# Kernel tuning notes

Hardware: AMD Instinct MI355X
Metric: run time of the kernel (lower is better)

Reference implementation:

```python
import jax, jax.numpy as jnp
import numpy as np

N = 50000   # nodes
E = 800000  # edges (avg degree 16)
D = 128     # feature dim
H = 4       # heads
DH = D // H # head dim


def setup_inputs() -> dict:
    key = jax.random.key(0)
    ks = jax.random.split(key, 12)
    s = 1.0 / np.sqrt(D)
    return {
        "x": jax.random.normal(ks[0], (N, D), dtype=jnp.float32),
        "src": jax.random.randint(ks[1], (E,), 0, N, dtype=jnp.int32),
        "dst": jax.random.randint(ks[2], (E,), 0, N, dtype=jnp.int32),
        # input_linear: Linear(d, d)
        "W_in": jax.random.uniform(ks[3], (D, D), jnp.float32, -s, s),
        "b_in": jax.random.uniform(ks[4], (D,), jnp.float32, -s, s),
        # attn_linear_u: Linear(d, n_heads), attn_linear_v: Linear(d, n_heads, bias=False)
        "W_au": jax.random.uniform(ks[5], (D, H), jnp.float32, -s, s),
        "b_au": jax.random.uniform(ks[6], (H,), jnp.float32, -s, s),
        "W_av": jax.random.uniform(ks[7], (D, H), jnp.float32, -s, s),
        # FFN: Linear(d, d) -> ReLU -> Linear(d, d)  (dropout=0)
        "W_f1": jax.random.uniform(ks[8], (D, D), jnp.float32, -s, s),
        "b_f1": jax.random.uniform(ks[9], (D,), jnp.float32, -s, s),
        "W_f2": jax.random.uniform(ks[10], (D, D), jnp.float32, -s, s),
        "b_f2": jax.random.uniform(ks[11], (D,), jnp.float32, -s, s),
    }


def reference(x, src, dst, W_in, b_in, W_au, b_au, W_av, W_f1, b_f1, W_f2, b_f2):
    h = x @ W_in + b_in                                # [N, D]
    su = h @ W_au + b_au                               # [N, H]
    sv = h @ W_av                                      # [N, H]
    # u_add_v gather + LeakyReLU
    e = jax.nn.leaky_relu(su[src] + sv[dst], 0.2)      # [E, H]
    # edge_softmax: softmax over incoming edges of each dst node
    m = jax.ops.segment_max(e, dst, num_segments=N)    # [N, H]
    ex = jnp.exp(e - m[dst])                           # [E, H]
    z = jax.ops.segment_sum(ex, dst, num_segments=N)   # [N, H]
    p = ex / z[dst]                                    # [E, H]
    # u_mul_e_sum: weighted aggregation (note reshape order (N, d_head, H))
    hu = h.reshape(N, DH, H)[src]                      # [E, DH, H]
    agg = jax.ops.segment_sum(hu * p[:, None, :], dst, num_segments=N)  # [N, DH, H]
    y = agg.reshape(N, D)
    # FFN
    return jax.nn.relu(y @ W_f1 + b_f1) @ W_f2 + b_f2
```

## Files before the change

kernel.cpp:

```cpp
#include <hip/hip_runtime.h>
#include <hip/hip_bf16.h>
#include <math.h>

#define D 128
#define NHEADS 4

static constexpr int CAP  = 64;
static constexpr int CAPB = 5120;
static constexpr int EB   = 4096;

typedef __attribute__((ext_vector_type(8))) short bf16x8;
typedef __attribute__((ext_vector_type(4))) float f32x4;

__device__ __forceinline__ float4 ld4(const float* p) {
    return *reinterpret_cast<const float4*>(p);
}
__device__ __forceinline__ float4 fma4(float a, float4 b, float4 c) {
    c.x = fmaf(a, b.x, c.x); c.y = fmaf(a, b.y, c.y);
    c.z = fmaf(a, b.z, c.z); c.w = fmaf(a, b.w, c.w);
    return c;
}
__device__ __forceinline__ unsigned short f2bf(float f) {
    __hip_bfloat16 b = __float2bfloat16(f);
    return __builtin_bit_cast(unsigned short, b);
}
__device__ __forceinline__ float bf2f(unsigned short u) {
    return __uint_as_float((unsigned)u << 16);
}
__device__ __forceinline__ void cvt_hilo(const float4& a0, const float4& a1,
                                         bf16x8& hi, bf16x8& lo) {
    float v[8] = {a0.x, a0.y, a0.z, a0.w, a1.x, a1.y, a1.z, a1.w};
#pragma unroll
    for (int i = 0; i < 8; ++i) {
        unsigned short h = f2bf(v[i]);
        hi[i] = (short)h;
        lo[i] = (short)f2bf(v[i] - bf2f(h));
    }
}

template<int MODE>
__global__ __launch_bounds__(256)
void mfma_gemm128(const float* __restrict__ A, const float* __restrict__ W,
                  const float* __restrict__ bias, float* __restrict__ out,
                  unsigned short* __restrict__ out16, int N, int ntiles,
                  const float* __restrict__ Wau, const float* __restrict__ bau,
                  const float* __restrict__ Wav,
                  float* __restrict__ su, float* __restrict__ sv)
{
    __shared__ unsigned short wh[D * D];
    __shared__ unsigned short wl[D * D];

    const int t = threadIdx.x;
#pragma unroll
    for (int i = 0; i < 16; ++i) {
        int g = t + i * 256;
        int col = g & 127;
        int k0 = (g >> 7) << 2;
        short4 h4, l4;
#pragma unroll
        for (int k = 0; k < 4; ++k) {
            float v = W[(size_t)(k0 + k) * D + col];
            unsigned short hb = f2bf(v);
            ((short*)&h4)[k] = (short)hb;
            ((short*)&l4)[k] = (short)f2bf(v - bf2f(hb));
        }
        int off = col * D + (k0 ^ ((col & 7) << 3));
        *reinterpret_cast<short4*>(&wh[off]) = h4;
        *reinterpret_cast<short4*>(&wl[off]) = l4;
    }
    __syncthreads();

    const int wid  = t >> 6;
    const int lane = t & 63;
    const int q8   = (lane >> 4) * 8;

    float4 bau4 = {0, 0, 0, 0};
    if constexpr (MODE == 0) bau4 = ld4(bau);

    for (int tile = blockIdx.x; tile < ntiles; tile += gridDim.x) {
        const int rbase = tile * 64 + wid * 16;
        const int arow  = rbase + (lane & 15);

        bf16x8 ahi[4], alo[4];
#pragma unroll
        for (int ks = 0; ks < 4; ++ks) {
            float4 a0 = {0, 0, 0, 0}, a1 = {0, 0, 0, 0};
            if (arow < N) {
                const float* ap = A + (size_t)arow * D + 32 * ks + q8;
                a0 = ld4(ap); a1 = ld4(ap + 4);
            }
            cvt_hilo(a0, a1, ahi[ks], alo[ks]);
        }

        f32x4 acc[8];
#pragma unroll
        for (int ct = 0; ct < 8; ++ct) acc[ct] = (f32x4){0.f, 0.f, 0.f, 0.f};

#pragma unroll
        for (int ct = 0; ct < 8; ++ct) {
            const int colb = ct * 16 + (lane & 15);
            const int sw   = (colb & 7) << 3;
            bf16x8 bh[4], bl[4];
#pragma unroll
            for (int ks = 0; ks < 4; ++ks) {
                int off = colb * D + ((32 * ks + q8) ^ sw);
                bh[ks] = *reinterpret_cast<const bf16x8*>(&wh[off]);
                bl[ks] = *reinterpret_cast<const bf16x8*>(&wl[off]);
            }
#pragma unroll
            for (int ks = 0; ks < 4; ++ks) {
                acc[ct] = __builtin_amdgcn_mfma_f32_16x16x32_bf16(ahi[ks], bh[ks], acc[ct], 0, 0, 0);
                acc[ct] = __builtin_amdgcn_mfma_f32_16x16x32_bf16(alo[ks], bh[ks], acc[ct], 0, 0, 0);
                acc[ct] = __builtin_amdgcn_mfma_f32_16x16x32_bf16(ahi[ks], bl[ks], acc[ct], 0, 0, 0);
            }
        }

        const int crow0 = rbase + (lane >> 4) * 4;

        float4 s_u[4], s_v[4];
        if constexpr (MODE == 0) {
#pragma unroll
            for (int j = 0; j < 4; ++j) { s_u[j] = {0,0,0,0}; s_v[j] = {0,0,0,0}; }
        }

#pragma unroll
        for (int ct = 0; ct < 8; ++ct) {
            const int col = ct * 16 + (lane & 15);
            const float bv = bias[col];
            float4 wau4, wav4;
            if constexpr (MODE == 0) {
                wau4 = ld4(Wau + col * NHEADS);
                wav4 = ld4(Wav + col * NHEADS);
            }
#pragma unroll
            for (int j = 0; j < 4; ++j) {
                const int r = crow0 + j;
                float v = acc[ct][j] + bv;
                if constexpr (MODE == 1) v = fmaxf(v, 0.f);
                if (r < N) {
                    if constexpr (MODE == 0)
                        out16[(size_t)r * D + col] = f2bf(v);
                    else
                        out[(size_t)r * D + col] = v;
                }
                if constexpr (MODE == 0) {
                    s_u[j] = fma4(v, wau4, s_u[j]);
                    s_v[j] = fma4(v, wav4, s_v[j]);
                }
            }
        }

        if constexpr (MODE == 0) {
#pragma unroll
            for (int j = 0; j < 4; ++j) {
#pragma unroll
                for (int d2 = 1; d2 < 16; d2 <<= 1) {
                    s_u[j].x += __shfl_xor(s_u[j].x, d2); s_u[j].y += __shfl_xor(s_u[j].y, d2);
                    s_u[j].z += __shfl_xor(s_u[j].z, d2); s_u[j].w += __shfl_xor(s_u[j].w, d2);
                    s_v[j].x += __shfl_xor(s_v[j].x, d2); s_v[j].y += __shfl_xor(s_v[j].y, d2);
                    s_v[j].z += __shfl_xor(s_v[j].z, d2); s_v[j].w += __shfl_xor(s_v[j].w, d2);
                }
            }
            if ((lane & 15) == 0) {
#pragma unroll
                for (int j = 0; j < 4; ++j) {
                    const int r = crow0 + j;
                    if (r < N) {
                        float4 u = s_u[j];
                        u.x += bau4.x; u.y += bau4.y; u.z += bau4.z; u.w += bau4.w;
                        *reinterpret_cast<float4*>(su + (size_t)r * NHEADS) = u;
                        *reinterpret_cast<float4*>(sv + (size_t)r * NHEADS) = s_v[j];
                    }
                }
            }
        }
    }
}

__global__ __launch_bounds__(256)
void bin_kernel(const int* __restrict__ src, const int* __restrict__ dst,
                int* __restrict__ bucket_cnt ,
                unsigned* __restrict__ bucket_buf, int E, int NB)
{
    __shared__ int hist[256];
    __shared__ int base[256];
    __shared__ int off[256];
    const int t = threadIdx.x;
    hist[t] = 0; off[t] = 0;
    __syncthreads();

    const int e0 = blockIdx.x * EB;
#pragma unroll
    for (int j = 0; j < EB / 256; ++j) {
        int idx = e0 + j * 256 + t;
        if (idx < E) atomicAdd(&hist[dst[idx] >> 8], 1);
    }
    __syncthreads();
    if (t < NB) {
        int hv = hist[t];
        base[t] = hv ? atomicAdd(&bucket_cnt[t * 16], hv) : 0;
    }
    __syncthreads();
#pragma unroll
    for (int j = 0; j < EB / 256; ++j) {
        int idx = e0 + j * 256 + t;
        if (idx < E) {
            int d = dst[idx];
            int b = d >> 8;
            int p = base[b] + atomicAdd(&off[b], 1);
            if (p < CAPB)
                bucket_buf[(size_t)b * CAPB + p] =
                    (unsigned)(src[idx] | ((d & 255) << 16));
        }
    }
}

__global__ __launch_bounds__(256)
void csr_kernel(const int* __restrict__ bucket_cnt, const unsigned* __restrict__ bucket_buf,
                unsigned short* __restrict__ slot, int* __restrict__ deg, int N)
{
    __shared__ unsigned ebuf[CAPB];
    __shared__ int cur[256];
    const int b = blockIdx.x;
    const int t = threadIdx.x;
    const int cnt = min(bucket_cnt[b * 16], CAPB);
    cur[t] = 0;
    for (int i = t; i < cnt; i += 256)
        ebuf[i] = bucket_buf[(size_t)b * CAPB + i];
    __syncthreads();
    for (int i = t; i < cnt; i += 256) {
        unsigned e = ebuf[i];
        int dl = e >> 16;
        int pos = atomicAdd(&cur[dl], 1);
        if (pos < CAP)
            slot[(((size_t)(b * 256 + dl)) << 6) + pos] = (unsigned short)(e & 0xffff);
    }
    __syncthreads();
    int n = b * 256 + t;
    if (n < N) deg[n] = min(cur[t], CAP);
}

__global__ __launch_bounds__(256)
void agg_kernel(const unsigned short* __restrict__ h16, const float* __restrict__ su,
                const float* __restrict__ sv, const int* __restrict__ deg_arr,
                const unsigned short* __restrict__ slot, float* __restrict__ y, int N)
{
    __shared__ int   s_s[4][64];
    __shared__ float s_p[4][64][4];

    const int wslot = threadIdx.x >> 6;
    const int lane  = threadIdx.x & 63;
    const int n = blockIdx.x * 4 + wslot;
    if (n >= N) return;

    const int deg = deg_arr[n];

    if (deg == 0) {
        *reinterpret_cast<float2*>(y + (size_t)n * D + lane * 2) = float2{0.f, 0.f};
        return;
    }

    const float4 sv4 = ld4(sv + (size_t)n * NHEADS);

    float4 z4 = {0.f, 0.f, 0.f, 0.f};
    float2 acc = {0.f, 0.f};
    const int psel = (lane & 1) * 2;

    int sj = 0;
    float4 ex4 = {0.f, 0.f, 0.f, 0.f};
    if (lane < deg) {
        sj = slot[((size_t)n << 6) + lane];
        float4 u = ld4(su + (size_t)sj * NHEADS);
        float e0 = u.x + sv4.x, e1 = u.y + sv4.y, e2 = u.z + sv4.z, e3 = u.w + sv4.w;
        e0 = e0 >= 0.f ? e0 : 0.2f * e0; e1 = e1 >= 0.f ? e1 : 0.2f * e1;
        e2 = e2 >= 0.f ? e2 : 0.2f * e2; e3 = e3 >= 0.f ? e3 : 0.2f * e3;
        ex4.x = __expf(e0); ex4.y = __expf(e1);
        ex4.z = __expf(e2); ex4.w = __expf(e3);
    }
    float4 tt = ex4;
#pragma unroll
    for (int d2 = 1; d2 < 64; d2 <<= 1) {
        tt.x += __shfl_xor(tt.x, d2); tt.y += __shfl_xor(tt.y, d2);
        tt.z += __shfl_xor(tt.z, d2); tt.w += __shfl_xor(tt.w, d2);
    }
    z4.x += tt.x; z4.y += tt.y; z4.z += tt.z; z4.w += tt.w;

    s_s[wslot][lane] = sj;
    *reinterpret_cast<float4*>(&s_p[wslot][lane][0]) = ex4;
    __builtin_amdgcn_wave_barrier();

#pragma unroll 4
    for (int j = 0; j < deg; ++j) {
        int s = s_s[wslot][j];
        float2 p2 = *reinterpret_cast<const float2*>(&s_p[wslot][j][psel]);
        unsigned u = *reinterpret_cast<const unsigned*>(h16 + ((size_t)s << 7) + (lane << 1));
        acc.x = fmaf(p2.x, __uint_as_float(u << 16), acc.x);
        acc.y = fmaf(p2.y, __uint_as_float(u & 0xffff0000u), acc.y);
    }

    const float2 z2 = (lane & 1) ? float2{z4.z, z4.w} : float2{z4.x, z4.y};
    float2 o;
    o.x = acc.x / z2.x;
    o.y = acc.y / z2.y;
    *reinterpret_cast<float2*>(y + (size_t)n * D + lane * 2) = o;
}

extern "C" void kernel_launch(void* const* d_in, const int* in_sizes, int n_in,
                              void* d_out, int out_size, void* d_ws, size_t ws_size,
                              hipStream_t stream) {
    const float* x    = (const float*)d_in[0];
    const int*   src  = (const int*)d_in[1];
    const int*   dst  = (const int*)d_in[2];
    const float* W_in = (const float*)d_in[3];
    const float* b_in = (const float*)d_in[4];
    const float* W_au = (const float*)d_in[5];
    const float* b_au = (const float*)d_in[6];
    const float* W_av = (const float*)d_in[7];
    const float* W_f1 = (const float*)d_in[8];
    const float* b_f1 = (const float*)d_in[9];
    const float* W_f2 = (const float*)d_in[10];
    const float* b_f2 = (const float*)d_in[11];
    float* out = (float*)d_out;

    const int N = in_sizes[0] / D;
    const int E = in_sizes[1];
    const int NB = (N + 255) / 256;

    char* ws = (char*)d_ws;
    size_t o = 0;
    auto alloc = [&](size_t bytes) -> void* {
        void* p = ws + o;
        o += (bytes + 255) & ~(size_t)255;
        return p;
    };
    void*           bufA       = alloc((size_t)N * D * 4);
    float*          y          = (float*)alloc((size_t)N * D * 4);
    float*          su         = (float*)alloc((size_t)N * NHEADS * 4);
    float*          sv         = (float*)alloc((size_t)N * NHEADS * 4);
    int*            bucket_cnt = (int*)alloc((size_t)NB * 16 * 4);
    unsigned*       bucket_buf = (unsigned*)alloc((size_t)NB * CAPB * 4);
    unsigned short* slot       = (unsigned short*)alloc((size_t)NB * 256 * CAP * 2);
    int*            deg        = (int*)alloc((size_t)N * 4);

    unsigned short* h16 = (unsigned short*)bufA;
    float*          hid = (float*)bufA;

    hipMemsetAsync(bucket_cnt, 0, (size_t)NB * 16 * 4, stream);

    const int ntiles = (N + 63) / 64;
    const int ggrid  = (ntiles + 1) / 2;
    const int bgrid  = (E + EB - 1) / EB;

    bin_kernel<<<bgrid, 256, 0, stream>>>(src, dst, bucket_cnt, bucket_buf, E, NB);

    mfma_gemm128<0><<<ggrid, 256, 0, stream>>>(x, W_in, b_in, nullptr, h16, N, ntiles,
                                               W_au, b_au, W_av, su, sv);

    csr_kernel<<<NB, 256, 0, stream>>>(bucket_cnt, bucket_buf, slot, deg, N);

    agg_kernel<<<(N + 3) / 4, 256, 0, stream>>>(h16, su, sv, deg, slot, y, N);

    mfma_gemm128<1><<<ggrid, 256, 0, stream>>>(y, W_f1, b_f1, hid, nullptr, N, ntiles,
                                               nullptr, nullptr, nullptr, nullptr, nullptr);
    mfma_gemm128<2><<<ggrid, 256, 0, stream>>>(hid, W_f2, b_f2, out, nullptr, N, ntiles,
                                               nullptr, nullptr, nullptr, nullptr, nullptr);
}
```

Baseline: 134.8 us.

## Precompute bf16 hi/lo weight splits once and split attention scores into separate kernel

```diff
diff --git a/kernel.cpp b/kernel.cpp
--- a/kernel.cpp
+++ b/kernel.cpp
@@ -38,18 +38,14 @@
     }
 }
 
-template<int MODE>
-__global__ __launch_bounds__(256)
-void mfma_gemm128(const float* __restrict__ A, const float* __restrict__ W,
-                  const float* __restrict__ bias, float* __restrict__ out,
-                  unsigned short* __restrict__ out16, int N, int ntiles,
-                  const float* __restrict__ Wau, const float* __restrict__ bau,
-                  const float* __restrict__ Wav,
-                  float* __restrict__ su, float* __restrict__ sv)
-{
-    __shared__ unsigned short wh[D * D];
-    __shared__ unsigned short wl[D * D];
-
+__global__ __launch_bounds__(256)
+void wprep_kernel(const float* __restrict__ W0, const float* __restrict__ W1,
+                  const float* __restrict__ W2, unsigned short* __restrict__ wpre)
+{
+    const float* Ws[3] = {W0, W1, W2};
+    const float* W = Ws[blockIdx.x];
+    unsigned short* oh = wpre + (size_t)blockIdx.x * 32768;
+    unsigned short* ol = oh + 16384;
     const int t = threadIdx.x;
 #pragma unroll
     for (int i = 0; i < 16; ++i) {
@@ -65,8 +61,31 @@
             ((short*)&l4)[k] = (short)f2bf(v - bf2f(hb));
         }
         int off = col * D + (k0 ^ ((col & 7) << 3));
-        *reinterpret_cast<short4*>(&wh[off]) = h4;
-        *reinterpret_cast<short4*>(&wl[off]) = l4;
+        *reinterpret_cast<short4*>(&oh[off]) = h4;
+        *reinterpret_cast<short4*>(&ol[off]) = l4;
+    }
+}
+
+template<int MODE>
+__global__ __launch_bounds__(256)
+void mfma_gemm128(const float* __restrict__ A, const unsigned short* __restrict__ wpre,
+                  const float* __restrict__ bias, float* __restrict__ out,
+                  unsigned short* __restrict__ out16, int N)
+{
+    __shared__ unsigned short wh[D * D];
+    __shared__ unsigned short wl[D * D];
+
+    const int t = threadIdx.x;
+    {
+        const float4* srcf = reinterpret_cast<const float4*>(wpre);
+        float4* dh = reinterpret_cast<float4*>(wh);
+        float4* dl = reinterpret_cast<float4*>(wl);
+#pragma unroll
+        for (int i = 0; i < 8; ++i) {
+            int idx = t + i * 256;
+            dh[idx] = srcf[idx];
+            dl[idx] = srcf[idx + 2048];
+        }
     }
     __syncthreads();
 
@@ -74,106 +93,97 @@
     const int lane = t & 63;
     const int q8   = (lane >> 4) * 8;
 
-    float4 bau4 = {0, 0, 0, 0};
-    if constexpr (MODE == 0) bau4 = ld4(bau);
-
-    for (int tile = blockIdx.x; tile < ntiles; tile += gridDim.x) {
-        const int rbase = tile * 64 + wid * 16;
-        const int arow  = rbase + (lane & 15);
-
-        bf16x8 ahi[4], alo[4];
+    const int rbase = blockIdx.x * 64 + wid * 16;
+    const int arow  = rbase + (lane & 15);
+
+    bf16x8 ahi[4], alo[4];
+#pragma unroll
+    for (int ks = 0; ks < 4; ++ks) {
+        float4 a0 = {0, 0, 0, 0}, a1 = {0, 0, 0, 0};
+        if (arow < N) {
+            const float* ap = A + (size_t)arow * D + 32 * ks + q8;
+            a0 = ld4(ap); a1 = ld4(ap + 4);
+        }
+        cvt_hilo(a0, a1, ahi[ks], alo[ks]);
+    }
+
+    f32x4 acc[8];
+#pragma unroll
+    for (int ct = 0; ct < 8; ++ct) acc[ct] = (f32x4){0.f, 0.f, 0.f, 0.f};
+
+#pragma unroll
+    for (int ct = 0; ct < 8; ++ct) {
+        const int colb = ct * 16 + (lane & 15);
+        const int sw   = (colb & 7) << 3;
+        bf16x8 bh[4], bl[4];
 #pragma unroll
         for (int ks = 0; ks < 4; ++ks) {
-            float4 a0 = {0, 0, 0, 0}, a1 = {0, 0, 0, 0};
-            if (arow < N) {
-                const float* ap = A + (size_t)arow * D + 32 * ks + q8;
-                a0 = ld4(ap); a1 = ld4(ap + 4);
-            }
-            cvt_hilo(a0, a1, ahi[ks], alo[ks]);
-        }
-
-        f32x4 acc[8];
-#pragma unroll
-        for (int ct = 0; ct < 8; ++ct) acc[ct] = (f32x4){0.f, 0.f, 0.f, 0.f};
-
-#pragma unroll
-        for (int ct = 0; ct < 8; ++ct) {
-            const int colb = ct * 16 + (lane & 15);
-            const int sw   = (colb & 7) << 3;
-            bf16x8 bh[4], bl[4];
-#pragma unroll
-            for (int ks = 0; ks < 4; ++ks) {
-                int off = colb * D + ((32 * ks + q8) ^ sw);
-                bh[ks] = *reinterpret_cast<const bf16x8*>(&wh[off]);
-                bl[ks] = *reinterpret_cast<const bf16x8*>(&wl[off]);
-            }
-#pragma unroll
-            for (int ks = 0; ks < 4; ++ks) {
-                acc[ct] = __builtin_amdgcn_mfma_f32_16x16x32_bf16(ahi[ks], bh[ks], acc[ct], 0, 0, 0);
-                acc[ct] = __builtin_amdgcn_mfma_f32_16x16x32_bf16(alo[ks], bh[ks], acc[ct], 0, 0, 0);
-                acc[ct] = __builtin_amdgcn_mfma_f32_16x16x32_bf16(ahi[ks], bl[ks], acc[ct], 0, 0, 0);
-            }
-        }
-
-        const int crow0 = rbase + (lane >> 4) * 4;
-
-        float4 s_u[4], s_v[4];
-        if constexpr (MODE == 0) {
-#pragma unroll
-            for (int j = 0; j < 4; ++j) { s_u[j] = {0,0,0,0}; s_v[j] = {0,0,0,0}; }
-        }
-
-#pragma unroll
-        for (int ct = 0; ct < 8; ++ct) {
-            const int col = ct * 16 + (lane & 15);
-            const float bv = bias[col];
-            float4 wau4, wav4;
-            if constexpr (MODE == 0) {
-                wau4 = ld4(Wau + col * NHEADS);
-                wav4 = ld4(Wav + col * NHEADS);
-            }
-#pragma unroll
-            for (int j = 0; j < 4; ++j) {
-                const int r = crow0 + j;
+            int off = colb * D + ((32 * ks + q8) ^ sw);
+            bh[ks] = *reinterpret_cast<const bf16x8*>(&wh[off]);
+            bl[ks] = *reinterpret_cast<const bf16x8*>(&wl[off]);
+        }
+#pragma unroll
+        for (int ks = 0; ks < 4; ++ks) {
+            acc[ct] = __builtin_amdgcn_mfma_f32_16x16x32_bf16(ahi[ks], bh[ks], acc[ct], 0, 0, 0);
+            acc[ct] = __builtin_amdgcn_mfma_f32_16x16x32_bf16(alo[ks], bh[ks], acc[ct], 0, 0, 0);
+            acc[ct] = __builtin_amdgcn_mfma_f32_16x16x32_bf16(ahi[ks], bl[ks], acc[ct], 0, 0, 0);
+        }
+    }
+
+    const int crow0 = rbase + (lane >> 4) * 4;
+#pragma unroll
+    for (int ct = 0; ct < 8; ++ct) {
+        const int col = ct * 16 + (lane & 15);
+        const float bv = bias[col];
+#pragma unroll
+        for (int j = 0; j < 4; ++j) {
+            const int r = crow0 + j;
+            if (r < N) {
                 float v = acc[ct][j] + bv;
                 if constexpr (MODE == 1) v = fmaxf(v, 0.f);
-                if (r < N) {
-                    if constexpr (MODE == 0)
-                        out16[(size_t)r * D + col] = f2bf(v);
-                    else
-                        out[(size_t)r * D + col] = v;
-                }
-                if constexpr (MODE == 0) {
-                    s_u[j] = fma4(v, wau4, s_u[j]);
-                    s_v[j] = fma4(v, wav4, s_v[j]);
-                }
+                if constexpr (MODE == 0)
+                    out16[(size_t)r * D + col] = f2bf(v);
+                else
+                    out[(size_t)r * D + col] = v;
             }
         }
-
-        if constexpr (MODE == 0) {
-#pragma unroll
-            for (int j = 0; j < 4; ++j) {
-#pragma unroll
-                for (int d2 = 1; d2 < 16; d2 <<= 1) {
-                    s_u[j].x += __shfl_xor(s_u[j].x, d2); s_u[j].y += __shfl_xor(s_u[j].y, d2);
-                    s_u[j].z += __shfl_xor(s_u[j].z, d2); s_u[j].w += __shfl_xor(s_u[j].w, d2);
-                    s_v[j].x += __shfl_xor(s_v[j].x, d2); s_v[j].y += __shfl_xor(s_v[j].y, d2);
-                    s_v[j].z += __shfl_xor(s_v[j].z, d2); s_v[j].w += __shfl_xor(s_v[j].w, d2);
-                }
-            }
-            if ((lane & 15) == 0) {
-#pragma unroll
-                for (int j = 0; j < 4; ++j) {
-                    const int r = crow0 + j;
-                    if (r < N) {
-                        float4 u = s_u[j];
-                        u.x += bau4.x; u.y += bau4.y; u.z += bau4.z; u.w += bau4.w;
-                        *reinterpret_cast<float4*>(su + (size_t)r * NHEADS) = u;
-                        *reinterpret_cast<float4*>(sv + (size_t)r * NHEADS) = s_v[j];
-                    }
-                }
-            }
-        }
+    }
+}
+
+__global__ __launch_bounds__(256)
+void att_scores_kernel(const unsigned short* __restrict__ h16,
+                       const float* __restrict__ Wau, const float* __restrict__ bau,
+                       const float* __restrict__ Wav,
+                       float* __restrict__ su, float* __restrict__ sv, int N)
+{
+    const int wid  = threadIdx.x >> 6;
+    const int lane = threadIdx.x & 63;
+    const int n = blockIdx.x * 4 + wid;
+    if (n >= N) return;
+
+    const int c = lane * 2;
+    unsigned u = *reinterpret_cast<const unsigned*>(h16 + (size_t)n * D + c);
+    const float hx = __uint_as_float(u << 16);
+    const float hy = __uint_as_float(u & 0xffff0000u);
+
+    float4 s_u = {0, 0, 0, 0}, s_v = {0, 0, 0, 0};
+    s_u = fma4(hx, ld4(Wau + c * NHEADS), s_u);
+    s_u = fma4(hy, ld4(Wau + (c + 1) * NHEADS), s_u);
+    s_v = fma4(hx, ld4(Wav + c * NHEADS), s_v);
+    s_v = fma4(hy, ld4(Wav + (c + 1) * NHEADS), s_v);
+
+#pragma unroll
+    for (int d2 = 1; d2 < 64; d2 <<= 1) {
+        s_u.x += __shfl_xor(s_u.x, d2); s_u.y += __shfl_xor(s_u.y, d2);
+        s_u.z += __shfl_xor(s_u.z, d2); s_u.w += __shfl_xor(s_u.w, d2);
+        s_v.x += __shfl_xor(s_v.x, d2); s_v.y += __shfl_xor(s_v.y, d2);
+        s_v.z += __shfl_xor(s_v.z, d2); s_v.w += __shfl_xor(s_v.w, d2);
+    }
+    if (lane == 0) {
+        float4 ub = ld4(bau);
+        s_u.x += ub.x; s_u.y += ub.y; s_u.z += ub.z; s_u.w += ub.w;
+        *reinterpret_cast<float4*>(su + (size_t)n * NHEADS) = s_u;
+        *reinterpret_cast<float4*>(sv + (size_t)n * NHEADS) = s_v;
     }
 }
 
@@ -341,6 +351,7 @@
     unsigned*       bucket_buf = (unsigned*)alloc((size_t)NB * CAPB * 4);
     unsigned short* slot       = (unsigned short*)alloc((size_t)NB * 256 * CAP * 2);
     int*            deg        = (int*)alloc((size_t)N * 4);
+    unsigned short* wpre       = (unsigned short*)alloc((size_t)3 * 32768 * 2);
 
     unsigned short* h16 = (unsigned short*)bufA;
     float*          hid = (float*)bufA;
@@ -348,20 +359,20 @@
     hipMemsetAsync(bucket_cnt, 0, (size_t)NB * 16 * 4, stream);
 
     const int ntiles = (N + 63) / 64;
-    const int ggrid  = (ntiles + 1) / 2;
     const int bgrid  = (E + EB - 1) / EB;
 
+    wprep_kernel<<<3, 256, 0, stream>>>(W_in, W_f1, W_f2, wpre);
+
     bin_kernel<<<bgrid, 256, 0, stream>>>(src, dst, bucket_cnt, bucket_buf, E, NB);
 
-    mfma_gemm128<0><<<ggrid, 256, 0, stream>>>(x, W_in, b_in, nullptr, h16, N, ntiles,
-                                               W_au, b_au, W_av, su, sv);
+    mfma_gemm128<0><<<ntiles, 256, 0, stream>>>(x, wpre, b_in, nullptr, h16, N);
 
     csr_kernel<<<NB, 256, 0, stream>>>(bucket_cnt, bucket_buf, slot, deg, N);
 
+    att_scores_kernel<<<(N + 3) / 4, 256, 0, stream>>>(h16, W_au, b_au, W_av, su, sv, N);
+
     agg_kernel<<<(N + 3) / 4, 256, 0, stream>>>(h16, su, sv, deg, slot, y, N);
 
-    mfma_gemm128<1><<<ggrid, 256, 0, stream>>>(y, W_f1, b_f1, hid, nullptr, N, ntiles,
-                                               nullptr, nullptr, nullptr, nullptr, nullptr);
-    mfma_gemm128<2><<<ggrid, 256, 0, stream>>>(hid, W_f2, b_f2, out, nullptr, N, ntiles,
-                                               nullptr, nullptr, nullptr, nullptr, nullptr);
-}
+    mfma_gemm128<1><<<ntiles, 256, 0, stream>>>(y, wpre + 32768, b_f1, hid, nullptr, N);
+    mfma_gemm128<2><<<ntiles, 256, 0, stream>>>(hid, wpre + 65536, b_f2, out, nullptr, N);
+}
```

Measured after the change: 168.8 us. 25.2% more time.
